# Kernel tuning notes

Measured on AMD Instinct MI355X. Metric: run time of the kernel, lower is better.

Reference implementation:

```python
import jax, jax.numpy as jnp
import numpy as np

WS, OWS, NH, DIM, MLP_H = 16, 24, 6, 180, 360
PAD = (OWS - WS) // 2
SCALE = (DIM // NH) ** -0.5


def _ln(x, w, b):
    m = jnp.mean(x, -1, keepdims=True)
    v = jnp.var(x, -1, keepdims=True)
    return (x - m) * jax.lax.rsqrt(v + 1e-5) * w + b


def _rpi():
    # relative position index between ordinary (WS) and extended (OWS) windows
    ci = np.stack(np.meshgrid(np.arange(WS), np.arange(WS), indexing='ij')).reshape(2, -1)
    ce = np.stack(np.meshgrid(np.arange(OWS), np.arange(OWS), indexing='ij')).reshape(2, -1)
    rel = (ce[:, None, :] - ci[:, :, None]).transpose(1, 2, 0) + (WS - 1)  # [WS^2, OWS^2, 2]
    rel[:, :, 0] *= WS + OWS - 1
    return jnp.asarray(rel.sum(-1), dtype=jnp.int32)  # values in [0, (WS+OWS-1)^2)


def setup_inputs():
    key = jax.random.key(0)
    ks = jax.random.split(key, 8)
    h = w = 256
    b = 1
    p = lambda k, shape: jax.random.normal(k, shape, jnp.float32) * 0.02
    return {
        'x': jax.random.normal(ks[0], (b, h * w, DIM), jnp.float32),
        'rpi': _rpi(),
        'norm1_w': jnp.ones((DIM,), jnp.float32), 'norm1_b': jnp.zeros((DIM,), jnp.float32),
        'qkv_w': p(ks[1], (DIM, 3 * DIM)), 'qkv_b': jnp.zeros((3 * DIM,), jnp.float32),
        'rpb': p(ks[2], ((WS + OWS - 1) ** 2, NH)),
        'proj_w': p(ks[3], (DIM, DIM)), 'proj_b': jnp.zeros((DIM,), jnp.float32),
        'norm2_w': jnp.ones((DIM,), jnp.float32), 'norm2_b': jnp.zeros((DIM,), jnp.float32),
        'fc1_w': p(ks[4], (DIM, MLP_H)), 'fc1_b': jnp.zeros((MLP_H,), jnp.float32),
        'fc2_w': p(ks[5], (MLP_H, DIM)), 'fc2_b': jnp.zeros((DIM,), jnp.float32),
        'h': h, 'w': w,
    }


def _ocab(x, rpi, norm1_w, norm1_b, qkv_w, qkv_b, rpb, proj_w, proj_b,
          norm2_w, norm2_b, fc1_w, fc1_b, fc2_w, fc2_b, h, w):
    b, L, c = x.shape
    nhw, nww = h // WS, w // WS
    nw = nhw * nww
    shortcut = x
    xn = _ln(x, norm1_w, norm1_b).reshape(b, h, w, c)
    qkv = xn @ qkv_w + qkv_b                      # [b,h,w,3c]
    q = qkv[..., :c]
    kv = jnp.moveaxis(qkv[..., c:], -1, 1)        # [b,2c,h,w]
    # non-overlapping query windows -> [b*nw, WS*WS, c]
    qw = q.reshape(b, nhw, WS, nww, WS, c).transpose(0, 1, 3, 2, 4, 5).reshape(b * nw, WS * WS, c)
    # overlapping KV windows (torch.nn.Unfold(kernel=OWS, stride=WS, pad=PAD) equivalent)
    kv_pad = jnp.pad(kv, ((0, 0), (0, 0), (PAD, PAD), (PAD, PAD)))
    rows = (jnp.arange(nhw) * WS)[:, None] + jnp.arange(OWS)   # [nhw, OWS]
    cols = (jnp.arange(nww) * WS)[:, None] + jnp.arange(OWS)   # [nww, OWS]
    kvw = kv_pad[:, :, rows][:, :, :, :, cols]    # [b,2c,nhw,OWS,nww,OWS]
    kvw = kvw.reshape(b, 2, c, nhw, OWS, nww, OWS)
    kvw = kvw.transpose(1, 0, 3, 5, 4, 6, 2).reshape(2, b * nw, OWS * OWS, c)
    k_w, v_w = kvw[0], kvw[1]
    B_, nq, n, d = b * nw, WS * WS, OWS * OWS, c // NH
    q_ = qw.reshape(B_, nq, NH, d).transpose(0, 2, 1, 3) * SCALE
    k_ = k_w.reshape(B_, n, NH, d).transpose(0, 2, 1, 3)
    v_ = v_w.reshape(B_, n, NH, d).transpose(0, 2, 1, 3)
    attn = jnp.einsum('bhqd,bhnd->bhqn', q_, k_)
    bias = rpb[rpi.reshape(-1)].reshape(nq, n, NH).transpose(2, 0, 1)  # [NH, nq, n]
    attn = jax.nn.softmax(attn + bias[None], axis=-1)
    out = jnp.einsum('bhqn,bhnd->bhqd', attn, v_).transpose(0, 2, 1, 3).reshape(B_, nq, c)
    # window reverse
    out = out.reshape(b, nhw, nww, WS, WS, c).transpose(0, 1, 3, 2, 4, 5).reshape(b, h * w, c)
    x = out @ proj_w + proj_b + shortcut
    xn2 = _ln(x, norm2_w, norm2_b)
    mlp = jax.nn.gelu(xn2 @ fc1_w + fc1_b, approximate=False) @ fc2_w + fc2_b
    return x + mlp


def reference(x, rpi, norm1_w, norm1_b, qkv_w, qkv_b, rpb, proj_w, proj_b,
              norm2_w, norm2_b, fc1_w, fc1_b, fc2_w, fc2_b, h, w):
    return _ocab(x, rpi, norm1_w, norm1_b, qkv_w, qkv_b, rpb, proj_w, proj_b,
                 norm2_w, norm2_b, fc1_w, fc1_b, fc2_w, fc2_b, h, w)
```

## Files before the change

### kernel.cpp

```cpp
#include <hip/hip_runtime.h>

typedef float f32x4 __attribute__((ext_vector_type(4)));
typedef float fvec4 __attribute__((ext_vector_type(4)));
typedef __bf16 bf16x8 __attribute__((ext_vector_type(8)));
typedef unsigned short u16;
typedef u16 u16x8 __attribute__((ext_vector_type(8)));
typedef u16 u16x4 __attribute__((ext_vector_type(4)));
typedef int i32x2 __attribute__((ext_vector_type(2)));

#define SCALE_Q 0.18257418583505536f
#define LOG2E   1.4426950408889634f
#define SCALE_Q2 (SCALE_Q * LOG2E)

__device__ __forceinline__ u16 f2bf(float f) {
    union { __bf16 h; u16 u; } cv; cv.h = (__bf16)f; return cv.u;
}
__device__ __forceinline__ float bf2f(u16 u) {
    union { __bf16 h; u16 u; } cv; cv.u = u; return (float)cv.h;
}
__device__ __forceinline__ float exp2_raw(float x) {
    float r;
    asm("v_exp_f32 %0, %1" : "=v"(r) : "v"(x));
    return r;
}
__device__ __forceinline__ unsigned pk_bf16(float a, float b) {
    unsigned r;
    asm("v_cvt_pk_bf16_f32 %0, %1, %2" : "=v"(r) : "v"(a), "v"(b));
    return r;
}

#define GLD16(gsrc, ldst) __builtin_amdgcn_global_load_lds( \
    (const __attribute__((address_space(1))) unsigned*)(gsrc), \
    (__attribute__((address_space(3))) unsigned*)(ldst), 16, 0, 0)

__device__ __forceinline__ void xswap16(int a, int b, int& u, int& v) {
#if __has_builtin(__builtin_amdgcn_permlane16_swap)
    i32x2 r = __builtin_amdgcn_permlane16_swap(a, b, false, false);
    u = r[0]; v = r[1];
#else
    int sa = __builtin_amdgcn_ds_swizzle(a, 0x401F);
    int sb = __builtin_amdgcn_ds_swizzle(b, 0x401F);
    bool hi = (threadIdx.x & 16) != 0;
    u = hi ? sb : a;
    v = hi ? b : sa;
#endif
}

__device__ __forceinline__ void border_yx(int i, int& y, int& x) {
    if (i < 1056)      { y = i / 264; x = i % 264; }
    else if (i < 2112) { int j = i - 1056; y = 260 + j / 264; x = j % 264; }
    else               { int j = i - 2112; y = 4 + (j >> 3); int xx = j & 7;
                         x = (xx < 4) ? xx : 256 + xx; }
}

__global__ __launch_bounds__(256)
void prepln_k(const float* __restrict__ x, const float* __restrict__ n1w,
              const float* __restrict__ n1b, u16* __restrict__ xn,
              const float* __restrict__ qkv_w, const float* __restrict__ proj_w,
              const float* __restrict__ fc1_w, const float* __restrict__ fc2_w,
              const int* __restrict__ rpi, const float* __restrict__ rpb,
              u16* __restrict__ qkvT, u16* __restrict__ projT,
              u16* __restrict__ fc1T, u16* __restrict__ fc2T,
              u16* __restrict__ bias5, unsigned* __restrict__ kp_u32,
              unsigned* __restrict__ vp_u32)
{
    if (blockIdx.x < 16384) {
        int row = blockIdx.x * 4 + (threadIdx.x >> 6);
        int lane = threadIdx.x & 63;
        fvec4 v = {0.f, 0.f, 0.f, 0.f};
        if (lane < 45) v = *(const fvec4*)(x + (long)row * 180 + lane * 4);
        float s  = v.x + v.y + v.z + v.w;
        float sq = v.x * v.x + v.y * v.y + v.z * v.z + v.w * v.w;
        for (int m = 1; m < 64; m <<= 1) { s += __shfl_xor(s, m); sq += __shfl_xor(sq, m); }
        float mean = s * (1.f / 180.f);
        float var  = sq * (1.f / 180.f) - mean * mean;
        float rstd = rsqrtf(var + 1e-5f);
        if (lane < 45) {
            u16x4 o;
            #pragma unroll
            for (int j = 0; j < 4; j++) {
                int c = lane * 4 + j;
                o[j] = f2bf((v[j] - mean) * rstd * n1w[c] + n1b[c]);
            }
            *(u16x4*)(xn + (long)row * 192 + lane * 4) = o;
        } else if (lane < 48) {
            u16x4 z = {0, 0, 0, 0};
            *(u16x4*)(xn + (long)row * 192 + 180 + (lane - 45) * 4) = z;
        }
        return;
    }
    int idx = (blockIdx.x - 16384) * 256 + threadIdx.x;
    if (idx < 122880) {
        int e = idx & 7, l15b = (idx >> 3) & 15, lgb = (idx >> 7) & 3;
        int kstep = (idx >> 9) % 6, ng = idx / 3072;
        int col = ng * 16 + l15b, kd = kstep * 32 + lgb * 8 + e;
        qkvT[idx] = (col < 540 && kd < 180) ? f2bf(qkv_w[kd * 540 + col]) : (u16)0;
    } else if (idx < 172032) {
        int i = idx - 122880;
        int e = i & 7, l15b = (i >> 3) & 15, lgb = (i >> 7) & 3;
        int kstep = (i >> 9) % 6, ng = i / 3072;
        int col = ng * 16 + l15b, kd = kstep * 32 + lgb * 8 + e;
        projT[i] = (col < 180 && kd < 180) ? f2bf(proj_w[kd * 180 + col]) : (u16)0;
    } else if (idx < 245760) {
        int i = idx - 172032;
        int e = i & 7, l15b = (i >> 3) & 15, lgb = (i >> 7) & 3;
        int kstep = (i >> 9) % 6, ng = i / 3072;
        int col = ng * 16 + l15b, kd = kstep * 32 + lgb * 8 + e;
        fc1T[i] = (col < 360 && kd < 180) ? f2bf(fc1_w[kd * 360 + col]) : (u16)0;
    } else if (idx < 344064) {
        int i = idx - 245760;
        int e = i & 7, l15b = (i >> 3) & 15, lgb = (i >> 7) & 3;
        int kstep = (i >> 9) % 12, ng = i / 6144;
        int col = ng * 16 + l15b, kd = kstep * 32 + lgb * 8 + e;
        fc2T[i] = (col < 180 && kd < 360) ? f2bf(fc2_w[kd * 180 + col]) : (u16)0;
    } else if (idx < 1228800) {
        int i = idx - 344064;
        int e = i & 15, l15 = (i >> 4) & 15, wv2 = (i >> 8) & 3, lg2 = (i >> 10) & 3;
        int cm36 = i >> 12;
        int hh = cm36 / 36, cm = cm36 % 36;
        int ch = cm >> 2, mi = cm & 3;
        int ni = e >> 2, rr = e & 3;
        int q = wv2 * 64 + ni * 16 + l15;
        int key = ch * 64 + mi * 16 + lg2 * 4 + rr;
        bias5[i] = f2bf(rpb[rpi[q * 576 + key] * 6 + hh] * LOG2E);
    } else if (idx < 1628160) {
        int i = idx - 1228800;
        int tok = i >> 4, wj = i & 15;
        int h = tok / 4160, b = tok % 4160, y, xx;
        border_yx(b, y, xx);
        kp_u32[((h * 264 + y) * 264 + xx) * 16 + wj] = 0u;
    } else if (idx < 2021376) {
        int i = idx - 1628160;
        int h = i / 65536, t = i % 65536;
        int y = t >> 8, xx = t & 255;
        kp_u32[((h * 264 + y + 4) * 264 + xx + 4) * 16 + 15] = 0u;
    } else if (idx < 2236800) {
        int i = idx - 2021376;
        int h = i / 35904, r = i % 35904;
        vp_u32[(h * 32 + 30) * 35904 + r] = 0x3F803F80u;
    } else if (idx < 2452224) {
        int i = idx - 2236800;
        int h = i / 35904, r = i % 35904;
        vp_u32[(h * 32 + 31) * 35904 + r] = 0u;
    } else if (idx < 3016704) {
        int i = idx - 2452224;
        int hd = i / 3136, j = i % 3136;
        int h = hd / 30, d = hd % 30;
        int y, xu;
        if (j < 1088) { int r = j / 136; y = r + (r >= 4 ? 256 : 0); xu = j % 136; }
        else { int j2 = j - 1088; y = 4 + (j2 >> 3); int q = j2 & 7;
               xu = (q < 2) ? q : 128 + q; }
        vp_u32[((h * 32 + d) * 264 + y) * 136 + xu] = 0u;
    }
}

__global__ __launch_bounds__(256)
void lnb_k(const u16* __restrict__ in, const float* __restrict__ w,
           const float* __restrict__ b, u16* __restrict__ out)
{
    int row = blockIdx.x * 4 + (threadIdx.x >> 6);
    int lane = threadIdx.x & 63;
    fvec4 v = {0.f, 0.f, 0.f, 0.f};
    if (lane < 45) {
        u16x4 raw = *(const u16x4*)(in + (long)row * 192 + lane * 4);
        #pragma unroll
        for (int j = 0; j < 4; j++) v[j] = bf2f(raw[j]);
    }
    float s  = v.x + v.y + v.z + v.w;
    float sq = v.x * v.x + v.y * v.y + v.z * v.z + v.w * v.w;
    for (int m = 1; m < 64; m <<= 1) { s += __shfl_xor(s, m); sq += __shfl_xor(sq, m); }
    float mean = s * (1.f / 180.f);
    float var  = sq * (1.f / 180.f) - mean * mean;
    float rstd = rsqrtf(var + 1e-5f);
    if (lane < 45) {
        u16x4 o;
        #pragma unroll
        for (int j = 0; j < 4; j++) {
            int c = lane * 4 + j;
            o[j] = f2bf((v[j] - mean) * rstd * w[c] + b[c]);
        }
        *(u16x4*)(out + (long)row * 192 + lane * 4) = o;
    } else if (lane < 48) {
        u16x4 z = {0, 0, 0, 0};
        *(u16x4*)(out + (long)row * 192 + 180 + (lane - 45) * 4) = z;
    }
}

template<int KTOT, int NCB, int EPI>
__global__ __launch_bounds__(256)
void gemm_k(const u16* __restrict__ A, const u16* __restrict__ BtF,
            const float* __restrict__ bias, const float* __restrict__ resid,
            void* __restrict__ o0, void* __restrict__ o1, void* __restrict__ o2)
{
    constexpr int NH = KTOT / 192;
    constexpr int NKT = KTOT / 32;
    constexpr int AC = (NH == 1) ? 1 : NCB;
    __shared__ u16 lds_a[128 * 192];
    const int tid = threadIdx.x;
    const int l = tid & 63, wv = tid >> 6;
    const int wm = wv >> 1, wn = wv & 1;
    const int l15 = l & 15, lg = l >> 4;
    const int rx7 = l15 & 7;
    const long rowb = (long)blockIdx.x * 128;
    const int cb0 = blockIdx.y * NCB;
    const f32x4 fz = {0.f, 0.f, 0.f, 0.f};

    f32x4 acc[AC][4][2];
    #pragma unroll
    for (int a2 = 0; a2 < AC; a2++)
        #pragma unroll
        for (int i = 0; i < 4; i++) { acc[a2][i][0] = fz; acc[a2][i][1] = fz; }

    const u16* aptr[4];
    #pragma unroll
    for (int mi = 0; mi < 4; mi++)
        aptr[mi] = lds_a + (wm * 64 + mi * 16 + l15) * 192;

    auto epilogue = [&](int cb, f32x4 (&ac)[4][2]) {
        #pragma unroll
        for (int nd = 0; nd < 2; nd++) {
            const int c = cb * 64 + wn * 32 + nd * 16 + l15;
            if (EPI == 0) {
                if (c < 540) {
                    const float bb = bias[c];
                    const int sec = (c >= 360) ? 2 : ((c >= 180) ? 1 : 0);
                    const int cc = c - sec * 180;
                    const int hh = cc / 30, d = cc - hh * 30;
                    #pragma unroll
                    for (int mi = 0; mi < 4; mi++) {
                        const long t0 = rowb + wm * 64 + mi * 16 + lg * 4;
                        const int y = (int)(t0 >> 8), x0 = (int)(t0 & 255);
                        if (sec == 0) {
                            int win = ((y >> 4) << 4) | (x0 >> 4);
                            int qrow0 = ((y & 15) << 4) | (x0 & 15);
                            u16* dst = (u16*)o0 + (((long)(win * 6 + hh)) * 256 + qrow0) * 32 + d;
                            #pragma unroll
                            for (int rr = 0; rr < 4; rr++)
                                dst[rr * 32] = f2bf((ac[mi][nd][rr] + bb) * SCALE_Q2);
                        } else if (sec == 1) {
                            u16* dst = (u16*)o1 + (((long)hh * 264 + y + 4) * 264 + x0 + 4) * 32 + d;
                            #pragma unroll
                            for (int rr = 0; rr < 4; rr++)
                                dst[rr * 32] = f2bf(ac[mi][nd][rr] + bb);
                        } else {
                            long dstoff = (((long)hh * 32 + d) * 264 + y + 4) * 272 + x0 + 4;
                            union { u16x4 v4; unsigned u2[2]; } pv;
                            pv.u2[0] = pk_bf16(ac[mi][nd][0] + bb, ac[mi][nd][1] + bb);
                            pv.u2[1] = pk_bf16(ac[mi][nd][2] + bb, ac[mi][nd][3] + bb);
                            *(u16x4*)((u16*)o2 + dstoff) = pv.v4;
                        }
                    }
                }
            } else if (EPI == 1) {
                if (c < 180) {
                    const float bb = bias[c];
                    #pragma unroll
                    for (int mi = 0; mi < 4; mi++) {
                        const long t0 = rowb + wm * 64 + mi * 16 + lg * 4;
                        const float* rs = resid + t0 * 180 + c;
                        u16* dst = (u16*)o0 + t0 * 192 + c;
                        #pragma unroll
                        for (int rr = 0; rr < 4; rr++)
                            dst[rr * 192] = f2bf(ac[mi][nd][rr] + bb + rs[rr * 180]);
                    }
                }
            } else if (EPI == 2) {
                const float bb = (c < 360) ? bias[c] : 0.f;
                #pragma unroll
                for (int mi = 0; mi < 4; mi++) {
                    const long t0 = rowb + wm * 64 + mi * 16 + lg * 4;
                    u16* dst = (u16*)o0 + t0 * 384 + c;
                    #pragma unroll
                    for (int rr = 0; rr < 4; rr++) {
                        float xx = ac[mi][nd][rr] + bb;
                        float u2n = -2.f * xx * (0.7978845608f + 0.0356774081f * xx * xx);
                        dst[rr * 384] = f2bf(xx / (1.f + __expf(u2n)));
                    }
                }
            } else {
                if (c < 180) {
                    const float bb = bias[c];
                    const u16* x2b = (const u16*)o1;
                    #pragma unroll
                    for (int mi = 0; mi < 4; mi++) {
                        const long t0 = rowb + wm * 64 + mi * 16 + lg * 4;
                        const u16* rs = x2b + t0 * 192 + c;
                        float* dst = (float*)o0 + t0 * 180 + c;
                        #pragma unroll
                        for (int rr = 0; rr < 4; rr++)
                            dst[rr * 180] = ac[mi][nd][rr] + bb + bf2f(rs[rr * 192]);
                    }
                }
            }
        }
    };

    #pragma unroll
    for (int hk = 0; hk < NH; ++hk) {
        if (hk) __syncthreads();
        #pragma unroll
        for (int R = 0; R < 12; ++R) {
            int idx = R * 256 + tid;
            int row = idx / 24, gp = idx - row * 24;
            int g = (gp & 24) | ((gp & 7) ^ (row & 7));
            GLD16(A + (rowb + row) * KTOT + hk * 192 + g * 8,
                  (char*)lds_a + R * 4096 + wv * 1024);
        }
        __syncthreads();

        #pragma unroll
        for (int icb = 0; icb < NCB; ++icb) {
            f32x4 (&ac)[4][2] = acc[(NH == 1) ? 0 : icb];
            const u16* Bf = BtF + ((long)((cb0 + icb) * 4 + wn * 2) * NKT + hk * 6) * 512 + l * 8;
            #pragma unroll
            for (int kg = 0; kg < 6; kg += 3) {
                bf16x8 bfr[2][3];
                #pragma unroll
                for (int g2 = 0; g2 < 3; ++g2) {
                    bfr[0][g2] = *(const bf16x8*)(Bf + (kg + g2) * 512);
                    bfr[1][g2] = *(const bf16x8*)(Bf + (NKT + kg + g2) * 512);
                }
                #pragma unroll
                for (int g2 = 0; g2 < 3; ++g2) {
                    const int k = kg + g2;
                    const int gk = k * 4 + lg;
                    const int gpk = (gk & 24) | ((gk & 7) ^ rx7);
                    bf16x8 af[4];
                    #pragma unroll
                    for (int mi = 0; mi < 4; mi++)
                        af[mi] = *(const bf16x8*)(aptr[mi] + gpk * 8);
                    #pragma unroll
                    for (int mi = 0; mi < 4; mi++)
                        #pragma unroll
                        for (int nd = 0; nd < 2; nd++)
                            ac[mi][nd] = __builtin_amdgcn_mfma_f32_16x16x32_bf16(af[mi], bfr[nd][g2], ac[mi][nd], 0, 0, 0);
                }
            }
            if (NH == 1) {
                epilogue(cb0 + icb, ac);
                #pragma unroll
                for (int i = 0; i < 4; i++) { ac[i][0] = fz; ac[i][1] = fz; }
            }
        }
    }
    if (NH == 2) {
        #pragma unroll
        for (int icb = 0; icb < NCB; ++icb) epilogue(cb0 + icb, acc[icb]);
    }
}

__global__ __launch_bounds__(256)
void attn_k(const u16* __restrict__ q_g, const u16* __restrict__ K_pad,
            const u16* __restrict__ vP, const u16* __restrict__ bias5,
            u16* __restrict__ attn_out)
{
    __shared__ u16 kc[2][64 * 32];
    __shared__ u16 vt[2][32 * 64];

    const int w = ((blockIdx.x & 7) << 5) | (blockIdx.x >> 3);
    const int h = blockIdx.y;
    const int wy = w >> 4, wx = w & 15;
    const int tid = threadIdx.x;
    const int wv = tid >> 6, l = tid & 63;
    const int l15 = l & 15, lg = l >> 4;
    const int swzk = (l15 >> 1) & 3;
    const int swzv = l15 & 7;

    bf16x8 qb[4];
    #pragma unroll
    for (int ni = 0; ni < 4; ni++) {
        int qrow = wv * 64 + ni * 16 + l15;
        qb[ni] = *(const bf16x8*)(q_g + (((long)(w * 6 + h)) * 256 + qrow) * 32 + lg * 8);
    }

    f32x4 acc[2][4];
    #pragma unroll
    for (int i = 0; i < 2; i++)
        #pragma unroll
        for (int j = 0; j < 4; j++) acc[i][j] = (f32x4){0.f, 0.f, 0.f, 0.f};

    const int tK = tid >> 2;
    const int gtk = (l & 3) ^ ((l >> 3) & 3);
    const int aK = (tK >= 48) ? 2 : (tK >= 24 ? 1 : 0);
    const int bK = tK - aK * 24;
    const u16* KbaseRow = K_pad + (((long)(h * 264 + wy * 16)) * 264 + wx * 16) * 32 + gtk * 8;
    const int dV = tid >> 3;
    const int gtv = (l & 7) ^ (l >> 3);
    const int aV = gtv / 3, bV = (gtv % 3) * 8;
    const u16* Vrow0 = vP + ((((long)h * 32 + dV) * 264) + wy * 16) * 272 + wx * 16;
    const u16* Bp = bias5 + (long)h * 147456 + ((lg * 4 + wv) * 16 + l15) * 16;

    GLD16(KbaseRow + ((long)aK * 264 + bK) * 32, (char*)kc[0] + wv * 1024);
    GLD16(Vrow0 + aV * 272 + bV, (char*)vt[0] + wv * 1024);

    u16x8 bl[4], bh[4];
    #pragma unroll
    for (int mi = 0; mi < 4; mi++) {
        bl[mi] = *(const u16x8*)(Bp + mi * 4096);
        bh[mi] = *(const u16x8*)(Bp + mi * 4096 + 8);
    }

    #pragma unroll
    for (int ch = 0; ch < 9; ++ch) {
        __syncthreads();
        u16x8 bln[4], bhn[4];
        if (ch < 8) {
            int n = (ch + 1) * 64;
            int c1 = n / 24, c2 = n - c1 * 24;
            int bb2 = bK + c2;
            int t2 = bb2 >= 24;
            int oy = c1 + aK + t2, ox = bb2 - (t2 ? 24 : 0);
            GLD16(KbaseRow + ((long)oy * 264 + ox) * 32, (char*)kc[(ch + 1) & 1] + wv * 1024);
            int bbv = bV + c2;
            int t2v = bbv >= 24;
            int oyv = c1 + aV + t2v, oxv = bbv - (t2v ? 24 : 0);
            GLD16(Vrow0 + oyv * 272 + oxv, (char*)vt[(ch + 1) & 1] + wv * 1024);
            #pragma unroll
            for (int mi = 0; mi < 4; mi++) {
                bln[mi] = *(const u16x8*)(Bp + ((ch + 1) * 4 + mi) * 4096);
                bhn[mi] = *(const u16x8*)(Bp + ((ch + 1) * 4 + mi) * 4096 + 8);
            }
        }
        const u16* kcur = kc[ch & 1];
        const u16* vcur = vt[ch & 1];

        #pragma unroll
        for (int ks = 0; ks < 2; ++ks) {
            int Wp[2][4][2];
            #pragma unroll
            for (int mih = 0; mih < 2; ++mih) {
                int mi = ks * 2 + mih;
                int key = ks * 32 + mih * 16 + l15;
                bf16x8 ka = *(const bf16x8*)(kcur + key * 32 + (lg ^ swzk) * 8);
                union { u16x8 v; unsigned d[4]; } ulo, uhi;
                ulo.v = bl[mi]; uhi.v = bh[mi];
                f32x4 s[4];
                #pragma unroll
                for (int ni = 0; ni < 4; ni++) {
                    unsigned dA = (ni < 2) ? ulo.d[(ni & 1) * 2]     : uhi.d[(ni & 1) * 2];
                    unsigned dB = (ni < 2) ? ulo.d[(ni & 1) * 2 + 1] : uhi.d[(ni & 1) * 2 + 1];
                    f32x4 ci;
                    ci[0] = __uint_as_float(dA << 16);
                    ci[1] = __uint_as_float(dA & 0xFFFF0000u);
                    ci[2] = __uint_as_float(dB << 16);
                    ci[3] = __uint_as_float(dB & 0xFFFF0000u);
                    s[ni] = ci;
                }
                #pragma unroll
                for (int ni = 0; ni < 4; ni++)
                    s[ni] = __builtin_amdgcn_mfma_f32_16x16x32_bf16(ka, qb[ni], s[ni], 0, 0, 0);
                #pragma unroll
                for (int ni = 0; ni < 4; ni++) {
                    float p0 = exp2_raw(s[ni][0]);
                    float p1 = exp2_raw(s[ni][1]);
                    float p2 = exp2_raw(s[ni][2]);
                    float p3 = exp2_raw(s[ni][3]);
                    Wp[mih][ni][0] = (int)pk_bf16(p0, p1);
                    Wp[mih][ni][1] = (int)pk_bf16(p2, p3);
                }
            }
            bf16x8 va0 = *(const bf16x8*)(vcur + l15 * 64 + ((ks * 4 + lg) ^ swzv) * 8);
            bf16x8 va1 = *(const bf16x8*)(vcur + (16 + l15) * 64 + ((ks * 4 + lg) ^ swzv) * 8);
            #pragma unroll
            for (int ni = 0; ni < 4; ni++) {
                i32x2 r0 = __builtin_amdgcn_permlane32_swap(Wp[0][ni][0], Wp[1][ni][0], false, false);
                i32x2 r1 = __builtin_amdgcn_permlane32_swap(Wp[0][ni][1], Wp[1][ni][1], false, false);
                int wd0, wd1, wd2, wd3;
                xswap16(r0[0], r0[1], wd0, wd2);
                xswap16(r1[0], r1[1], wd1, wd3);
                union { int wd[4]; bf16x8 v; } pu;
                pu.wd[0] = wd0; pu.wd[1] = wd1; pu.wd[2] = wd2; pu.wd[3] = wd3;
                acc[0][ni] = __builtin_amdgcn_mfma_f32_16x16x32_bf16(va0, pu.v, acc[0][ni], 0, 0, 0);
                acc[1][ni] = __builtin_amdgcn_mfma_f32_16x16x32_bf16(va1, pu.v, acc[1][ni], 0, 0, 0);
            }
        }
        if (ch < 8) {
            #pragma unroll
            for (int mi = 0; mi < 4; mi++) { bl[mi] = bln[mi]; bh[mi] = bhn[mi]; }
        }
    }

    #pragma unroll
    for (int ni = 0; ni < 4; ni++) {
        float sum = __shfl(acc[1][ni][2], 48 + l15);
        float inv = 1.f / sum;
        int q = wv * 64 + ni * 16 + l15;
        int y = wy * 16 + (q >> 4), x = wx * 16 + (q & 15);
        u16* bp = attn_out + ((long)(y * 256 + x)) * 192 + h * 30;
        unsigned w0 = pk_bf16(acc[0][ni][0] * inv, acc[0][ni][1] * inv);
        unsigned w1 = pk_bf16(acc[0][ni][2] * inv, acc[0][ni][3] * inv);
        *(unsigned*)(bp + lg * 4)     = w0;
        *(unsigned*)(bp + lg * 4 + 2) = w1;
        unsigned w2 = pk_bf16(acc[1][ni][0] * inv, acc[1][ni][1] * inv);
        if (lg < 3) {
            unsigned w3 = pk_bf16(acc[1][ni][2] * inv, acc[1][ni][3] * inv);
            *(unsigned*)(bp + 16 + lg * 4)     = w2;
            *(unsigned*)(bp + 16 + lg * 4 + 2) = w3;
        } else {
            *(unsigned*)(bp + 28) = w2;
        }
    }
}

extern "C" void kernel_launch(void* const* d_in, const int* in_sizes, int n_in,
                              void* d_out, int out_size, void* d_ws, size_t ws_size,
                              hipStream_t stream)
{
    (void)in_sizes; (void)n_in; (void)out_size; (void)ws_size;
    const float* x      = (const float*)d_in[0];
    const int*   rpi    = (const int*)d_in[1];
    const float* n1w    = (const float*)d_in[2];
    const float* n1b    = (const float*)d_in[3];
    const float* qkv_w  = (const float*)d_in[4];
    const float* qkv_b  = (const float*)d_in[5];
    const float* rpb    = (const float*)d_in[6];
    const float* proj_w = (const float*)d_in[7];
    const float* proj_b = (const float*)d_in[8];
    const float* n2w    = (const float*)d_in[9];
    const float* n2b    = (const float*)d_in[10];
    const float* fc1_w  = (const float*)d_in[11];
    const float* fc1_b  = (const float*)d_in[12];
    const float* fc2_w  = (const float*)d_in[13];
    const float* fc2_b  = (const float*)d_in[14];
    float* out = (float*)d_out;

    char* ws = (char*)d_ws;
    size_t off = 0;
    auto alloc = [&](size_t bytes) -> void* {
        void* p = ws + off; off += (bytes + 511) & ~(size_t)511; return p;
    };
    u16*   xn     = (u16*)alloc(65536ull * 192 * 2);
    u16*   q_g    = (u16*)alloc(65536ull * 192 * 2);
    u16*   K_pad  = (u16*)alloc(6ull * 264 * 264 * 32 * 2);
    u16*   x2b    = (u16*)alloc(65536ull * 192 * 2);
    u16*   vP     = (u16*)alloc(6ull * 32 * 264 * 272 * 2);
    u16*   bias5  = (u16*)alloc(6ull * 36 * 4 * 4 * 16 * 16 * 2);
    u16*   qkvT   = (u16*)alloc(640ull * 192 * 2);
    u16*   projT  = (u16*)alloc(256ull * 192 * 2);
    u16*   fc1T   = (u16*)alloc(384ull * 192 * 2);
    u16*   fc2T   = (u16*)alloc(256ull * 384 * 2);
    u16*   ao     = xn;
    u16*   h1     = q_g;

    prepln_k<<<dim3(28168), dim3(256), 0, stream>>>(x, n1w, n1b, xn,
        qkv_w, proj_w, fc1_w, fc2_w, rpi, rpb,
        qkvT, projT, fc1T, fc2T, bias5, (unsigned*)K_pad, (unsigned*)vP);
    gemm_k<192, 3, 0><<<dim3(512, 3), dim3(256), 0, stream>>>(
        xn, qkvT, qkv_b, (const float*)nullptr, q_g, K_pad, vP);
    attn_k<<<dim3(256, 6), dim3(256), 0, stream>>>(q_g, K_pad, vP, bias5, ao);
    gemm_k<192, 3, 1><<<dim3(512, 1), dim3(256), 0, stream>>>(
        ao, projT, proj_b, x, x2b, nullptr, nullptr);
    lnb_k<<<dim3(16384), dim3(256), 0, stream>>>(x2b, n2w, n2b, xn);
    gemm_k<192, 3, 2><<<dim3(512, 2), dim3(256), 0, stream>>>(
        xn, fc1T, fc1_b, (const float*)nullptr, h1, nullptr, nullptr);
    gemm_k<384, 3, 3><<<dim3(512, 1), dim3(256), 0, stream>>>(
        h1, fc2T, fc2_b, (const float*)nullptr, out, x2b, nullptr);
}
```

Baseline: 248.0 us.

## Fuse fc1, GELU and fc2 into one MLP kernel keeping hidden activations in LDS

Replaces the separate fc1 GEMM (writing a bf16 hidden tensor to global memory) and fc2 GEMM with a single mlp_k kernel. Each block handles 64 rows, computes fc1 plus GELU into a swizzled LDS buffer, then runs fc2 from LDS and adds bias and residual. This removes the global round trip of the 65536x384 hidden tensor and one launch. The cost is 72KB of LDS per block, which may limit occupancy, and a smaller M tile per block. gemm_k is simplified to its single-K-pass path now that no caller uses KTOT=384.

```diff
diff --git a/kernel.cpp b/kernel.cpp
--- a/kernel.cpp
+++ b/kernel.cpp
@@ -192,9 +192,7 @@
             const float* __restrict__ bias, const float* __restrict__ resid,
             void* __restrict__ o0, void* __restrict__ o1, void* __restrict__ o2)
 {
-    constexpr int NH = KTOT / 192;
     constexpr int NKT = KTOT / 32;
-    constexpr int AC = (NH == 1) ? 1 : NCB;
     __shared__ u16 lds_a[128 * 192];
     const int tid = threadIdx.x;
     const int l = tid & 63, wv = tid >> 6;
@@ -205,11 +203,9 @@
     const int cb0 = blockIdx.y * NCB;
     const f32x4 fz = {0.f, 0.f, 0.f, 0.f};
 
-    f32x4 acc[AC][4][2];
-    #pragma unroll
-    for (int a2 = 0; a2 < AC; a2++)
-        #pragma unroll
-        for (int i = 0; i < 4; i++) { acc[a2][i][0] = fz; acc[a2][i][1] = fz; }
+    f32x4 acc[4][2];
+    #pragma unroll
+    for (int i = 0; i < 4; i++) { acc[i][0] = fz; acc[i][1] = fz; }
 
     const u16* aptr[4];
     #pragma unroll
@@ -251,7 +247,7 @@
                         }
                     }
                 }
-            } else if (EPI == 1) {
+            } else {
                 if (c < 180) {
                     const float bb = bias[c];
                     #pragma unroll
@@ -264,88 +260,147 @@
                             dst[rr * 192] = f2bf(ac[mi][nd][rr] + bb + rs[rr * 180]);
                     }
                 }
-            } else if (EPI == 2) {
-                const float bb = (c < 360) ? bias[c] : 0.f;
+            }
+        }
+    };
+
+    #pragma unroll
+    for (int R = 0; R < 12; ++R) {
+        int idx = R * 256 + tid;
+        int row = idx / 24, gp = idx - row * 24;
+        int g = (gp & 24) | ((gp & 7) ^ (row & 7));
+        GLD16(A + (rowb + row) * KTOT + g * 8,
+              (char*)lds_a + R * 4096 + wv * 1024);
+    }
+    __syncthreads();
+
+    #pragma unroll
+    for (int icb = 0; icb < NCB; ++icb) {
+        const u16* Bf = BtF + ((long)((cb0 + icb) * 4 + wn * 2) * NKT) * 512 + l * 8;
+        #pragma unroll
+        for (int kg = 0; kg < 6; kg += 3) {
+            bf16x8 bfr[2][3];
+            #pragma unroll
+            for (int g2 = 0; g2 < 3; ++g2) {
+                bfr[0][g2] = *(const bf16x8*)(Bf + (kg + g2) * 512);
+                bfr[1][g2] = *(const bf16x8*)(Bf + (NKT + kg + g2) * 512);
+            }
+            #pragma unroll
+            for (int g2 = 0; g2 < 3; ++g2) {
+                const int k = kg + g2;
+                const int gk = k * 4 + lg;
+                const int gpk = (gk & 24) | ((gk & 7) ^ rx7);
+                bf16x8 af[4];
                 #pragma unroll
-                for (int mi = 0; mi < 4; mi++) {
-                    const long t0 = rowb + wm * 64 + mi * 16 + lg * 4;
-                    u16* dst = (u16*)o0 + t0 * 384 + c;
+                for (int mi = 0; mi < 4; mi++)
+                    af[mi] = *(const bf16x8*)(aptr[mi] + gpk * 8);
+                #pragma unroll
+                for (int mi = 0; mi < 4; mi++)
                     #pragma unroll
-                    for (int rr = 0; rr < 4; rr++) {
-                        float xx = ac[mi][nd][rr] + bb;
-                        float u2n = -2.f * xx * (0.7978845608f + 0.0356774081f * xx * xx);
-                        dst[rr * 384] = f2bf(xx / (1.f + __expf(u2n)));
-                    }
-                }
-            } else {
-                if (c < 180) {
-                    const float bb = bias[c];
-                    const u16* x2b = (const u16*)o1;
-                    #pragma unroll
-                    for (int mi = 0; mi < 4; mi++) {
-                        const long t0 = rowb + wm * 64 + mi * 16 + lg * 4;
-                        const u16* rs = x2b + t0 * 192 + c;
-                        float* dst = (float*)o0 + t0 * 180 + c;
-                        #pragma unroll
-                        for (int rr = 0; rr < 4; rr++)
-                            dst[rr * 180] = ac[mi][nd][rr] + bb + bf2f(rs[rr * 192]);
-                    }
-                }
-            }
-        }
-    };
-
-    #pragma unroll
-    for (int hk = 0; hk < NH; ++hk) {
-        if (hk) __syncthreads();
-        #pragma unroll
-        for (int R = 0; R < 12; ++R) {
-            int idx = R * 256 + tid;
-            int row = idx / 24, gp = idx - row * 24;
-            int g = (gp & 24) | ((gp & 7) ^ (row & 7));
-            GLD16(A + (rowb + row) * KTOT + hk * 192 + g * 8,
-                  (char*)lds_a + R * 4096 + wv * 1024);
-        }
-        __syncthreads();
-
-        #pragma unroll
-        for (int icb = 0; icb < NCB; ++icb) {
-            f32x4 (&ac)[4][2] = acc[(NH == 1) ? 0 : icb];
-            const u16* Bf = BtF + ((long)((cb0 + icb) * 4 + wn * 2) * NKT + hk * 6) * 512 + l * 8;
-            #pragma unroll
-            for (int kg = 0; kg < 6; kg += 3) {
-                bf16x8 bfr[2][3];
+                    for (int nd = 0; nd < 2; nd++)
+                        acc[mi][nd] = __builtin_amdgcn_mfma_f32_16x16x32_bf16(af[mi], bfr[nd][g2], acc[mi][nd], 0, 0, 0);
+            }
+        }
+        epilogue(cb0 + icb, acc);
+        #pragma unroll
+        for (int i = 0; i < 4; i++) { acc[i][0] = fz; acc[i][1] = fz; }
+    }
+}
+
+__global__ __launch_bounds__(256)
+void mlp_k(const u16* __restrict__ A, const u16* __restrict__ fc1T,
+           const u16* __restrict__ fc2T, const float* __restrict__ b1,
+           const float* __restrict__ b2, const u16* __restrict__ resid,
+           float* __restrict__ out)
+{
+    __shared__ u16 lds_a[64 * 192];
+    __shared__ u16 H[64 * 384];
+    const int tid = threadIdx.x;
+    const int l = tid & 63, wv = tid >> 6;
+    const int l15 = l & 15, lg = l >> 4;
+    const int rx7 = l15 & 7;
+    const long rowb = (long)blockIdx.x * 64;
+    const f32x4 fz = {0.f, 0.f, 0.f, 0.f};
+
+    #pragma unroll
+    for (int R = 0; R < 6; ++R) {
+        int idx = R * 256 + tid;
+        int row = idx / 24, gp = idx - row * 24;
+        int g = (gp & 24) | ((gp & 7) ^ (row & 7));
+        GLD16(A + (rowb + row) * 192 + g * 8, (char*)lds_a + R * 4096 + wv * 1024);
+    }
+    __syncthreads();
+
+    const u16* aptr[4];
+    #pragma unroll
+    for (int mi = 0; mi < 4; mi++)
+        aptr[mi] = lds_a + (mi * 16 + l15) * 192;
+
+    #pragma unroll
+    for (int cb = 0; cb < 6; ++cb) {
+        f32x4 ac[4] = {fz, fz, fz, fz};
+        const u16* Bf = fc1T + ((long)(cb * 4 + wv) * 6) * 512 + l * 8;
+        #pragma unroll
+        for (int k = 0; k < 6; ++k) {
+            bf16x8 bfr = *(const bf16x8*)(Bf + k * 512);
+            const int gk = k * 4 + lg;
+            const int gpk = (gk & 24) | ((gk & 7) ^ rx7);
+            bf16x8 af[4];
+            #pragma unroll
+            for (int mi = 0; mi < 4; mi++)
+                af[mi] = *(const bf16x8*)(aptr[mi] + gpk * 8);
+            #pragma unroll
+            for (int mi = 0; mi < 4; mi++)
+                ac[mi] = __builtin_amdgcn_mfma_f32_16x16x32_bf16(af[mi], bfr, ac[mi], 0, 0, 0);
+        }
+        const int c = cb * 64 + wv * 16 + l15;
+        const float bb = (c < 360) ? b1[c] : 0.f;
+        const int gC = c >> 3, cL = c & 7;
+        #pragma unroll
+        for (int mi = 0; mi < 4; mi++) {
+            #pragma unroll
+            for (int rr = 0; rr < 4; rr++) {
+                int row = mi * 16 + lg * 4 + rr;
+                float xx = ac[mi][rr] + bb;
+                float u2n = -2.f * xx * (0.7978845608f + 0.0356774081f * xx * xx);
+                float ge = xx / (1.f + __expf(u2n));
+                int gS = (gC & ~7) | ((gC & 7) ^ (row & 7));
+                H[row * 384 + gS * 8 + cL] = f2bf(ge);
+            }
+        }
+    }
+    __syncthreads();
+
+    #pragma unroll
+    for (int cb = 0; cb < 3; ++cb) {
+        f32x4 ac[4] = {fz, fz, fz, fz};
+        const u16* Bf = fc2T + ((long)(cb * 4 + wv) * 12) * 512 + l * 8;
+        #pragma unroll
+        for (int k = 0; k < 12; ++k) {
+            bf16x8 bfr = *(const bf16x8*)(Bf + k * 512);
+            const int gk = k * 4 + lg;
+            const int gS = (gk & ~7) | ((gk & 7) ^ rx7);
+            bf16x8 af[4];
+            #pragma unroll
+            for (int mi = 0; mi < 4; mi++)
+                af[mi] = *(const bf16x8*)(H + (mi * 16 + l15) * 384 + gS * 8);
+            #pragma unroll
+            for (int mi = 0; mi < 4; mi++)
+                ac[mi] = __builtin_amdgcn_mfma_f32_16x16x32_bf16(af[mi], bfr, ac[mi], 0, 0, 0);
+        }
+        const int c = cb * 64 + wv * 16 + l15;
+        if (c < 180) {
+            const float bb = b2[c];
+            #pragma unroll
+            for (int mi = 0; mi < 4; mi++) {
+                const long t0 = rowb + mi * 16 + lg * 4;
+                const u16* rs = resid + t0 * 192 + c;
+                float* dst = out + t0 * 180 + c;
                 #pragma unroll
-                for (int g2 = 0; g2 < 3; ++g2) {
-                    bfr[0][g2] = *(const bf16x8*)(Bf + (kg + g2) * 512);
-                    bfr[1][g2] = *(const bf16x8*)(Bf + (NKT + kg + g2) * 512);
-                }
-                #pragma unroll
-                for (int g2 = 0; g2 < 3; ++g2) {
-                    const int k = kg + g2;
-                    const int gk = k * 4 + lg;
-                    const int gpk = (gk & 24) | ((gk & 7) ^ rx7);
-                    bf16x8 af[4];
-                    #pragma unroll
-                    for (int mi = 0; mi < 4; mi++)
-                        af[mi] = *(const bf16x8*)(aptr[mi] + gpk * 8);
-                    #pragma unroll
-                    for (int mi = 0; mi < 4; mi++)
-                        #pragma unroll
-                        for (int nd = 0; nd < 2; nd++)
-                            ac[mi][nd] = __builtin_amdgcn_mfma_f32_16x16x32_bf16(af[mi], bfr[nd][g2], ac[mi][nd], 0, 0, 0);
-                }
-            }
-            if (NH == 1) {
-                epilogue(cb0 + icb, ac);
-                #pragma unroll
-                for (int i = 0; i < 4; i++) { ac[i][0] = fz; ac[i][1] = fz; }
-            }
-        }
-    }
-    if (NH == 2) {
-        #pragma unroll
-        for (int icb = 0; icb < NCB; ++icb) epilogue(cb0 + icb, acc[icb]);
+                for (int rr = 0; rr < 4; rr++)
+                    dst[rr * 180] = ac[mi][rr] + bb + bf2f(rs[rr * 192]);
+            }
+        }
     }
 }
 
@@ -540,7 +595,7 @@
     u16*   fc1T   = (u16*)alloc(384ull * 192 * 2);
     u16*   fc2T   = (u16*)alloc(256ull * 384 * 2);
     u16*   ao     = xn;
-    u16*   h1     = q_g;
+    u16*   xn2    = q_g;
 
     prepln_k<<<dim3(28168), dim3(256), 0, stream>>>(x, n1w, n1b, xn,
         qkv_w, proj_w, fc1_w, fc2_w, rpi, rpb,
@@ -550,9 +605,7 @@
     attn_k<<<dim3(256, 6), dim3(256), 0, stream>>>(q_g, K_pad, vP, bias5, ao);
     gemm_k<192, 3, 1><<<dim3(512, 1), dim3(256), 0, stream>>>(
         ao, projT, proj_b, x, x2b, nullptr, nullptr);
-    lnb_k<<<dim3(16384), dim3(256), 0, stream>>>(x2b, n2w, n2b, xn);
-    gemm_k<192, 3, 2><<<dim3(512, 2), dim3(256), 0, stream>>>(
-        xn, fc1T, fc1_b, (const float*)nullptr, h1, nullptr, nullptr);
-    gemm_k<384, 3, 3><<<dim3(512, 1), dim3(256), 0, stream>>>(
-        h1, fc2T, fc2_b, (const float*)nullptr, out, x2b, nullptr);
-}
+    lnb_k<<<dim3(16384), dim3(256), 0, stream>>>(x2b, n2w, n2b, xn2);
+    mlp_k<<<dim3(1024), dim3(256), 0, stream>>>(
+        xn2, fc1T, fc2T, fc1_b, fc2_b, x2b, out);
+}
```

After: 218.7 us. 11.8% less time.
